# Optimization experiments

Measured on AMD Instinct MI355X. Metric: run time of the kernel, lower is better.

## Reference

```python
import jax, jax.numpy as jnp
import numpy as np

P = 399   # number of unshared per-position Conv1d kernels
K = 5     # conv kernel width (padding=2, 'same')


def _conv_stage(x, W, b):
    """Locally-connected stage: a distinct Conv1d per position along the last axis.
    x: [B, Cin, T, P]; W: [P, Cout, Cin, K]; b: [P, Cout] -> [B, Cout, T, P]."""
    xt = jnp.transpose(x, (3, 0, 1, 2))  # [P, B, Cin, T]

    def one(xi, wi, bi):
        y = jax.lax.conv_general_dilated(xi, wi, (1,), [(2, 2)],
                                         dimension_numbers=('NCH', 'OIH', 'NCH'))
        return y + bi[None, :, None]

    y = jax.vmap(one)(xt, W, b)          # [P, B, Cout, T]
    return jnp.transpose(y, (1, 2, 3, 0))


def _maxpool(x):
    # MaxPool2d((10,1), stride=(3,1)) over [B, C, T, P]
    return jax.lax.reduce_window(x, -jnp.inf, jax.lax.max,
                                 (1, 1, 10, 1), (1, 1, 3, 1), 'VALID')


def setup_inputs() -> dict:
    key = jax.random.key(0)
    ks = jax.random.split(key, 32)
    B, T = 256, 365

    def rn(k, shape, scale):
        return jax.random.normal(k, shape, jnp.float32) * scale

    d = {}
    d['x'] = jax.random.normal(ks[0], (B, T, P), jnp.float32)
    d['x2'] = jax.random.normal(ks[1], (B, 1307), jnp.float32)
    # per-position conv weights (PyTorch Conv1d layout O,I,K, stacked over P)
    d['W1'] = rn(ks[2], (P, 3, 1, K), 0.3); d['b1'] = rn(ks[3], (P, 3), 0.05)
    d['W2'] = rn(ks[4], (P, 3, 3, K), 0.2); d['b2'] = rn(ks[5], (P, 3), 0.05)
    d['W3'] = rn(ks[6], (P, 3, 3, K), 0.2); d['b3'] = rn(ks[7], (P, 3), 0.05)
    d['W4'] = rn(ks[8], (P, 3, 3, K), 0.2); d['b4'] = rn(ks[9], (P, 3), 0.05)
    # self.layers: 1307 -> 700 -> 200 -> 100
    d['lW1'] = rn(ks[10], (1307, 700), 0.02); d['lb1'] = rn(ks[11], (700,), 0.01)
    d['lW2'] = rn(ks[12], (700, 200), 0.03);  d['lb2'] = rn(ks[13], (200,), 0.01)
    d['lW3'] = rn(ks[14], (200, 100), 0.05);  d['lb3'] = rn(ks[15], (100,), 0.01)
    # self.common_layers: 1297 -> 500 -> 100 -> 20
    d['cW1'] = rn(ks[16], (1297, 500), 0.02); d['cb1'] = rn(ks[17], (500,), 0.01)
    d['cW2'] = rn(ks[18], (500, 100), 0.04);  d['cb2'] = rn(ks[19], (100,), 0.01)
    d['cW3'] = rn(ks[20], (100, 20), 0.08);   d['cb3'] = rn(ks[21], (20,), 0.01)
    # last_layer: 20 -> 1
    d['fW'] = rn(ks[22], (20, 1), 0.2);       d['fb'] = rn(ks[23], (1,), 0.01)
    return d


def reference(x, x2, W1, b1, W2, b2, W3, b3, W4, b4,
              lW1, lb1, lW2, lb2, lW3, lb3,
              cW1, cb1, cW2, cb2, cW3, cb3, fW, fb):
    h = x[:, None, :, :]                       # [B, 1, T, P]
    for W, b in ((W1, b1), (W2, b2), (W3, b3), (W4, b4)):
        h = _maxpool(jax.nn.relu(_conv_stage(h, W, b)))
    enc1 = h.reshape(h.shape[0], -1)           # [B, 3*1*399] = [B, 1197]

    e = jax.nn.relu(x2 @ lW1 + lb1)
    e = jax.nn.relu(e @ lW2 + lb2)
    enc2 = e @ lW3 + lb3                       # [B, 100] (no ReLU on final Linear)

    c = jnp.concatenate([enc1, enc2], axis=1)  # [B, 1297]
    c = jax.nn.relu(c @ cW1 + cb1)
    c = jax.nn.relu(c @ cW2 + cb2)
    c = jax.nn.relu(c @ cW3 + cb3)
    return c @ fW + fb                         # [B, 1]
```

## Files before the change

kernel.cpp:

```cpp
#include <hip/hip_runtime.h>

#define PP 399
#define BB 256


template<int SEG>
__device__ __forceinline__ float xload(const float* __restrict__ inp, int idx) {
    if (SEG == 2) {
        int ic = idx < 364 ? idx : 364;
        float v = inp[(long)ic * PP];
        return (idx <= 364) ? v : 0.f;
    }
    return inp[(long)idx * PP];
}

template<int OFF>
__device__ __forceinline__ void s1_group(const float (&xv)[13],
    const float (&w1)[3][5], const float (&B1)[3],
    float (&A1)[3], float (&c0)[3])
{
#pragma unroll
    for (int co = 0; co < 3; ++co) {
        float a0 = B1[co], a1 = B1[co], a2 = B1[co];
#pragma unroll
        for (int t = 0; t < 5; ++t) {
            a0 = fmaf(xv[OFF + t],     w1[co][t], a0);
            a1 = fmaf(xv[OFF + 1 + t], w1[co][t], a1);
            a2 = fmaf(xv[OFF + 2 + t], w1[co][t], a2);
        }
        c0[co] = a0;
        A1[co] = fmaxf(fmaxf(a0, a1), a2);
    }
}

template<int P2>
__device__ __forceinline__ void s2_step(
    float (&fe)[3][4], const float (&e)[3],
    const float (&w2)[3][3][5], const float (&B2)[3],
    float (&A2a)[3], float (&A2b)[3], float (&A2c)[3], float (&A2cur)[3],
    float*& op, bool do_c2, bool do_emit)
{
    if (do_c2) {
        float c2v[3];
#pragma unroll
        for (int co = 0; co < 3; ++co) {
            float a = B2[co];
#pragma unroll
            for (int ci = 0; ci < 3; ++ci) {
                a = fmaf(fe[ci][0], w2[co][ci][0], a);
                a = fmaf(fe[ci][1], w2[co][ci][1], a);
                a = fmaf(fe[ci][2], w2[co][ci][2], a);
                a = fmaf(fe[ci][3], w2[co][ci][3], a);
                a = fmaf(e[ci],     w2[co][ci][4], a);
            }
            c2v[co] = a;
        }
        if (P2 == 0) {
#pragma unroll
            for (int co = 0; co < 3; ++co) { A2a[co] = A2b[co]; A2b[co] = A2c[co]; A2c[co] = A2cur[co]; }
            if (do_emit) {
#pragma unroll
                for (int co = 0; co < 3; ++co)
                    op[co * PP] = fmaxf(fmaxf(fmaxf(fmaxf(A2a[co], A2b[co]), A2c[co]), c2v[co]), 0.f);
                op += 3 * PP;
            }
#pragma unroll
            for (int co = 0; co < 3; ++co) A2cur[co] = c2v[co];
        } else {
#pragma unroll
            for (int co = 0; co < 3; ++co) A2cur[co] = fmaxf(A2cur[co], c2v[co]);
        }
    }
#pragma unroll
    for (int ci = 0; ci < 3; ++ci) {
        fe[ci][0] = fe[ci][1]; fe[ci][1] = fe[ci][2]; fe[ci][2] = fe[ci][3]; fe[ci][3] = e[ci];
    }
}

template<int P2>
__device__ __forceinline__ void emit_e(
    const float (&Aa)[3], const float (&Ab)[3], const float (&Ac)[3],
    const float (&c0)[3],
    float (&fe)[3][4],
    const float (&w2)[3][3][5], const float (&B2)[3],
    float (&A2a)[3], float (&A2b)[3], float (&A2c)[3], float (&A2cur)[3],
    float*& op, bool do_c2, bool do_emit)
{
    float e[3];
#pragma unroll
    for (int co = 0; co < 3; ++co)
        e[co] = fmaxf(fmaxf(fmaxf(fmaxf(Aa[co], Ab[co]), Ac[co]), c0[co]), 0.f);
    s2_step<P2>(fe, e, w2, B2, A2a, A2b, A2c, A2cur, op, do_c2, do_emit);
}

template<int SEG>
__device__ __forceinline__ void s12_body(
    const float* __restrict__ x,
    const float* __restrict__ W1, const float* __restrict__ b1,
    const float* __restrict__ W2, const float* __restrict__ b2,
    float* __restrict__ h2, int b, int p)
{
    constexpr int J0tab[4] = {0, 13, 25, 37};
    constexpr int j0 = J0tab[SEG];
    constexpr int j1 = J0tab[SEG + 1];
    constexpr int k0 = (SEG == 0) ? 0 : 3 * j0 - 2;
    constexpr int kend = (3 * j1 + 11 < 121) ? (3 * j1 + 11) : 121;
    constexpr int NGRP = kend - k0 + 1;
    constexpr int NS = NGRP / 3;
    constexpr int NREM = NGRP - 3 * NS;
    constexpr int c2start = (SEG == 0) ? 5 : (k0 + 7);
    constexpr int e2start = 3 * j0 + 14;
    constexpr int P2_0 = (SEG == 0) ? 1 : 2;
    constexpr int P2_1 = (SEG == 0) ? 2 : 0;
    constexpr int P2_2 = (SEG == 0) ? 0 : 1;

    float w1[3][5], B1[3];
    {
        const float* wp = W1 + (long)p * 15;
#pragma unroll
        for (int co = 0; co < 3; ++co) {
#pragma unroll
            for (int t = 0; t < 5; ++t) w1[co][t] = wp[co * 5 + t];
            B1[co] = b1[(long)p * 3 + co];
        }
    }
    float w2[3][3][5], B2[3];
    {
        const float* wp = W2 + (long)p * 45;
#pragma unroll
        for (int co = 0; co < 3; ++co) {
#pragma unroll
            for (int ci = 0; ci < 3; ++ci)
#pragma unroll
                for (int t = 0; t < 5; ++t) w2[co][ci][t] = wp[(co * 3 + ci) * 5 + t];
            B2[co] = b2[(long)p * 3 + co];
        }
    }

    const float* __restrict__ inp = x + (long)b * 365 * PP + p;
    float* op = h2 + ((long)b * 37 + j0) * 3 * PP + p;

    float xv[13];
#pragma unroll
    for (int s = 0; s < 13; ++s) {
        int idx = 3 * k0 - 2 + s;
        xv[s] = (idx >= 0) ? inp[(long)idx * PP] : 0.f;
    }

    float fe[3][4];
    float A1p[3][3];
    float A2a[3], A2b[3], A2c[3], A2cur[3];
#pragma unroll
    for (int ci = 0; ci < 3; ++ci)
#pragma unroll
        for (int s = 0; s < 4; ++s) fe[ci][s] = 0.f;
#pragma unroll
    for (int co = 0; co < 3; ++co) {
        A1p[0][co] = 0.f; A1p[1][co] = 0.f; A1p[2][co] = 0.f;
        A2a[co] = 0.f; A2b[co] = 0.f; A2c[co] = 0.f; A2cur[co] = 0.f;
    }

    for (int S = 0; S < NS; ++S) {
        int k = k0 + 3 * S;
        float q[9];
#pragma unroll
        for (int s = 0; s < 9; ++s)
            q[s] = xload<SEG>(inp, 3 * k + 11 + s);

        float A1c0[3], A1c1[3], A1c2[3], c0[3];

        s1_group<0>(xv, w1, B1, A1c0, c0);
        if (S >= 1)
            emit_e<P2_0>(A1p[0], A1p[1], A1p[2], c0, fe, w2, B2,
                         A2a, A2b, A2c, A2cur, op,
                         k >= c2start, k >= e2start);
        s1_group<3>(xv, w1, B1, A1c1, c0);
        if (S >= 1)
            emit_e<P2_1>(A1p[1], A1p[2], A1c0, c0, fe, w2, B2,
                         A2a, A2b, A2c, A2cur, op,
                         k + 1 >= c2start, k + 1 >= e2start);
        s1_group<6>(xv, w1, B1, A1c2, c0);
        if (S >= 1)
            emit_e<P2_2>(A1p[2], A1c0, A1c1, c0, fe, w2, B2,
                         A2a, A2b, A2c, A2cur, op,
                         k + 2 >= c2start, k + 2 >= e2start);

#pragma unroll
        for (int co = 0; co < 3; ++co) {
            A1p[0][co] = A1c0[co]; A1p[1][co] = A1c1[co]; A1p[2][co] = A1c2[co];
        }
        xv[0] = xv[9]; xv[1] = xv[10]; xv[2] = xv[11]; xv[3] = xv[12];
#pragma unroll
        for (int s = 0; s < 9; ++s) xv[4 + s] = q[s];
    }

    if constexpr (NREM >= 1) {
        int k = k0 + 3 * NS;
        float A1c0[3], c0[3];
        s1_group<0>(xv, w1, B1, A1c0, c0);
        emit_e<P2_0>(A1p[0], A1p[1], A1p[2], c0, fe, w2, B2,
                     A2a, A2b, A2c, A2cur, op,
                     k >= c2start, k >= e2start);
        if constexpr (NREM >= 2) {
            float A1c1[3];
            s1_group<3>(xv, w1, B1, A1c1, c0);
            emit_e<P2_1>(A1p[1], A1p[2], A1c0, c0, fe, w2, B2,
                         A2a, A2b, A2c, A2cur, op,
                         k + 1 >= c2start, k + 1 >= e2start);
        }
    }
    if constexpr (SEG == 2) {
        float ez[3] = {0.f, 0.f, 0.f};
        s2_step<0>(fe, ez, w2, B2, A2a, A2b, A2c, A2cur, op, true, true);
    }
}

template<int RELU_A>
__device__ __forceinline__ void gemm_tile(
    const float* __restrict__ A, const float* __restrict__ Wt,
    float* __restrict__ out, int K, int N, int lda, int ldo, int kchunk,
    int bx, int by, int bz)
{
    __shared__ float As[32][36];
    __shared__ float Bs[32][36];

    int tid = threadIdx.x;
    int ty  = tid >> 3;
    int tx4 = (tid & 7) * 4;
    int c0 = bx * 32;
    int m0 = by * 32;
    int k0 = bz * kchunk;
    int klim = min(K, k0 + kchunk);

    float4 acc = make_float4(0.f, 0.f, 0.f, 0.f);

    for (int kb = k0; kb < klim; kb += 32) {
#pragma unroll
        for (int j = 0; j < 4; ++j) {
            int kk = kb + tx4 + j;
            float v = (kk < klim) ? A[(long)(m0 + ty) * lda + kk] : 0.f;
            if (RELU_A) v = fmaxf(v, 0.f);
            As[ty][tx4 + j] = v;
        }
#pragma unroll
        for (int j = 0; j < 4; ++j) {
            int kk = kb + ty;
            int c = c0 + tx4 + j;
            Bs[ty][tx4 + j] = (kk < klim && c < N) ? Wt[(long)kk * N + c] : 0.f;
        }
        __syncthreads();
#pragma unroll
        for (int kk = 0; kk < 32; ++kk) {
            float a = As[ty][kk];
            float4 bv = *(const float4*)&Bs[kk][tx4];
            acc.x = fmaf(a, bv.x, acc.x);
            acc.y = fmaf(a, bv.y, acc.y);
            acc.z = fmaf(a, bv.z, acc.z);
            acc.w = fmaf(a, bv.w, acc.w);
        }
        __syncthreads();
    }

    long m = m0 + ty;
    if (c0 + tx4 + 0 < N) atomicAdd(&out[m * ldo + c0 + tx4 + 0], acc.x);
    if (c0 + tx4 + 1 < N) atomicAdd(&out[m * ldo + c0 + tx4 + 1], acc.y);
    if (c0 + tx4 + 2 < N) atomicAdd(&out[m * ldo + c0 + tx4 + 2], acc.z);
    if (c0 + tx4 + 3 < N) atomicAdd(&out[m * ldo + c0 + tx4 + 3], acc.w);
}

template<int RELU_A>
__global__ __launch_bounds__(256)
void gemm_atomic(const float* __restrict__ A, const float* __restrict__ Wt,
                 float* __restrict__ out, int K, int N, int lda, int ldo, int kchunk)
{
    gemm_tile<RELU_A>(A, Wt, out, K, N, lda, ldo, kchunk,
                      blockIdx.x, blockIdx.y, blockIdx.z);
}

__global__ __launch_bounds__(256)
void init_e1(float* __restrict__ e1, const float* __restrict__ lb1)
{
    int idx = blockIdx.x * 256 + threadIdx.x;
    if (idx < BB * 700) e1[idx] = lb1[idx % 700];
}

__global__ __launch_bounds__(256)
void d1_conv_s12_lw1(const float* __restrict__ x,
                     const float* __restrict__ W1, const float* __restrict__ b1,
                     const float* __restrict__ W2, const float* __restrict__ b2,
                     float* __restrict__ h2,
                     const float* __restrict__ x2, const float* __restrict__ lW1,
                     float* __restrict__ e1,
                     float* __restrict__ e2,  const float* __restrict__ lb2,
                     float* __restrict__ cbuf, const float* __restrict__ lb3,
                     float* __restrict__ c1,  const float* __restrict__ cb1,
                     float* __restrict__ c2,  const float* __restrict__ cb2,
                     float* __restrict__ c3b, const float* __restrict__ cb3)
{
    int blk = blockIdx.x;
    if (blk < 1197) {
        int seg = blk / 399;
        int bx  = blk - seg * 399;
        int gid = bx * 256 + threadIdx.x;
        int b = gid / PP;
        int p = gid - b * PP;
        if (seg == 0)      s12_body<0>(x, W1, b1, W2, b2, h2, b, p);
        else if (seg == 1) s12_body<1>(x, W1, b1, W2, b2, h2, b, p);
        else               s12_body<2>(x, W1, b1, W2, b2, h2, b, p);
    } else if (blk < 1197 + 1056) {
        int g = blk - 1197;
        int gx = g % 22;
        int gy = (g / 22) % 8;
        int gz = g / 176;
        gemm_tile<0>(x2, lW1, e1, 1307, 700, 1307, 700, 256, gx, gy, gz);
    } else {
        int idx = (blk - 2253) * 256 + threadIdx.x;
        if (idx < BB * 200) { e2[idx] = lb2[idx % 200]; return; }
        idx -= BB * 200;
        if (idx < BB * 100) { int m = idx / 100, c = idx % 100; cbuf[(long)m * 1297 + 1197 + c] = lb3[c]; return; }
        idx -= BB * 100;
        if (idx < BB * 500) { c1[idx] = cb1[idx % 500]; return; }
        idx -= BB * 500;
        if (idx < BB * 100) { c2[idx] = cb2[idx % 100]; return; }
        idx -= BB * 100;
        if (idx < BB * 20)  { c3b[idx] = cb3[idx % 20]; return; }
    }
}

template<int CIN>
struct Stage {
    float w[3][CIN][5];
    float b[3];
    float xw[CIN][5];
    float m1[3], m2[3], m3[3];
    int nin;
};

__device__ __forceinline__ void init_s3(Stage<3>& s, const float* __restrict__ Wt,
                                        const float* __restrict__ Bs, int p) {
    const float* wp = Wt + (long)p * 45;
#pragma unroll
    for (int co = 0; co < 3; ++co)
#pragma unroll
        for (int ci = 0; ci < 3; ++ci)
#pragma unroll
            for (int k = 0; k < 5; ++k)
                s.w[co][ci][k] = wp[(co * 3 + ci) * 5 + k];
#pragma unroll
    for (int co = 0; co < 3; ++co) s.b[co] = Bs[(long)p * 3 + co];
#pragma unroll
    for (int ci = 0; ci < 3; ++ci)
#pragma unroll
        for (int k = 0; k < 5; ++k) s.xw[ci][k] = 0.f;
#pragma unroll
    for (int co = 0; co < 3; ++co) { s.m1[co] = -1e30f; s.m2[co] = -1e30f; s.m3[co] = -1e30f; }
    s.nin = 0;
}

template<int CIN>
__device__ __forceinline__ bool feed(Stage<CIN>& s, const float* in, float* out) {
#pragma unroll
    for (int ci = 0; ci < CIN; ++ci) {
        s.xw[ci][0] = s.xw[ci][1];
        s.xw[ci][1] = s.xw[ci][2];
        s.xw[ci][2] = s.xw[ci][3];
        s.xw[ci][3] = s.xw[ci][4];
        s.xw[ci][4] = in[ci];
    }
    int t = s.nin - 2;
    s.nin++;
    if (t < 0) return false;

    float c[3];
#pragma unroll
    for (int co = 0; co < 3; ++co) {
        float a = s.b[co];
#pragma unroll
        for (int ci = 0; ci < CIN; ++ci)
#pragma unroll
            for (int k = 0; k < 5; ++k)
                a = fmaf(s.xw[ci][k], s.w[co][ci][k], a);
        c[co] = fmaxf(a, 0.f);
    }

    bool emit = false;
    int ph = t % 3;
    if (ph == 0) {
        if (t >= 9) {
#pragma unroll
            for (int co = 0; co < 3; ++co) out[co] = fmaxf(s.m1[co], c[co]);
            emit = true;
        }
#pragma unroll
        for (int co = 0; co < 3; ++co) {
            float a = fmaxf(s.m2[co], c[co]);
            float bb = fmaxf(s.m3[co], c[co]);
            s.m1[co] = a; s.m2[co] = bb; s.m3[co] = c[co];
        }
    } else {
#pragma unroll
        for (int co = 0; co < 3; ++co) {
            s.m1[co] = fmaxf(s.m1[co], c[co]);
            s.m2[co] = fmaxf(s.m2[co], c[co]);
            s.m3[co] = fmaxf(s.m3[co], c[co]);
        }
    }
    return emit;
}

__device__ __forceinline__ void s34_body(
    const float* __restrict__ h2,
    const float* __restrict__ W3, const float* __restrict__ b3,
    const float* __restrict__ W4, const float* __restrict__ b4,
    float* __restrict__ cbuf, int b, int p)
{
    Stage<3> s3, s4;
    init_s3(s3, W3, b3, p);
    init_s3(s4, W4, b4, p);

    const float* inp = h2 + (long)b * 37 * 3 * PP + p;
    float* o4 = cbuf + (long)b * 1297 + p;

    float v3[3], v4[3];
    float z[3] = {0.f, 0.f, 0.f};

    float r0[3], r1[3], r2[3], r3[3], r4[3];
#pragma unroll
    for (int ci = 0; ci < 3; ++ci) {
        r0[ci] = inp[(long)(0 * 3 + ci) * PP];
        r1[ci] = inp[(long)(1 * 3 + ci) * PP];
        r2[ci] = inp[(long)(2 * 3 + ci) * PP];
        r3[ci] = inp[(long)(3 * 3 + ci) * PP];
        r4[ci] = inp[(long)(4 * 3 + ci) * PP];
    }

    for (int i = 0; i < 39; ++i) {
        float nn[3];
        int i5 = i + 5;
#pragma unroll
        for (int ci = 0; ci < 3; ++ci)
            nn[ci] = (i5 < 37) ? inp[(long)(i5 * 3 + ci) * PP] : 0.f;
        if (feed(s3, r0, v3)) {
            if (feed(s4, v3, v4)) {
#pragma unroll
                for (int co = 0; co < 3; ++co) o4[co * PP] = v4[co];
            }
        }
#pragma unroll
        for (int ci = 0; ci < 3; ++ci) {
            r0[ci] = r1[ci]; r1[ci] = r2[ci]; r2[ci] = r3[ci]; r3[ci] = r4[ci]; r4[ci] = nn[ci];
        }
    }
    for (int r = 0; r < 2; ++r) {
        if (feed(s4, z, v4)) {
#pragma unroll
            for (int co = 0; co < 3; ++co) o4[co * PP] = v4[co];
        }
    }
}

__global__ __launch_bounds__(256)
void d2_conv_s34_lw2(const float* __restrict__ h2,
                     const float* __restrict__ W3, const float* __restrict__ b3,
                     const float* __restrict__ W4, const float* __restrict__ b4,
                     float* __restrict__ cbuf,
                     const float* __restrict__ e1, const float* __restrict__ lW2,
                     float* __restrict__ e2)
{
    int blk = blockIdx.x;
    if (blk < 399) {
        int gid = blk * 256 + threadIdx.x;
        int b = gid / PP;
        int p = gid - b * PP;
        s34_body(h2, W3, b3, W4, b4, cbuf, b, p);
    } else {
        int g = blk - 399;
        int gx = g % 7;
        int gy = (g / 7) % 8;
        int gz = g / 56;
        gemm_tile<1>(e1, lW2, e2, 700, 200, 700, 200, 128, gx, gy, gz);
    }
}

__global__ __launch_bounds__(256)
void d3_lw3_cw1a(const float* __restrict__ e2, const float* __restrict__ lW3,
                 float* __restrict__ cbuf,
                 const float* __restrict__ cW1, float* __restrict__ c1)
{
    int blk = blockIdx.x;
    if (blk < 128) {
        int gx = blk % 4;
        int gy = (blk / 4) % 8;
        int gz = blk / 32;
        gemm_tile<1>(e2, lW3, cbuf + 1197, 200, 100, 200, 1297, 64, gx, gy, gz);
    } else {
        int g = blk - 128;
        int gx = g % 16;
        int gy = (g / 16) % 8;
        int gz = g / 128;
        gemm_tile<0>(cbuf, cW1, c1, 1197, 500, 1297, 500, 200, gx, gy, gz);
    }
}

__global__ __launch_bounds__(64)
void final_kernel(const float* __restrict__ c3,
                  const float* __restrict__ fW,
                  const float* __restrict__ fb,
                  float* __restrict__ out)
{
    int m = blockIdx.x * 64 + threadIdx.x;
    if (m >= BB) return;
    float acc = fb[0];
#pragma unroll
    for (int k = 0; k < 20; ++k)
        acc = fmaf(fmaxf(c3[m * 20 + k], 0.f), fW[k], acc);
    out[m] = acc;
}

extern "C" void kernel_launch(void* const* d_in, const int* in_sizes, int n_in,
                              void* d_out, int out_size, void* d_ws, size_t ws_size,
                              hipStream_t stream)
{
    const float* x   = (const float*)d_in[0];
    const float* x2  = (const float*)d_in[1];
    const float* W1  = (const float*)d_in[2];
    const float* b1  = (const float*)d_in[3];
    const float* W2  = (const float*)d_in[4];
    const float* b2  = (const float*)d_in[5];
    const float* W3  = (const float*)d_in[6];
    const float* b3  = (const float*)d_in[7];
    const float* W4  = (const float*)d_in[8];
    const float* b4  = (const float*)d_in[9];
    const float* lW1 = (const float*)d_in[10];
    const float* lb1 = (const float*)d_in[11];
    const float* lW2 = (const float*)d_in[12];
    const float* lb2 = (const float*)d_in[13];
    const float* lW3 = (const float*)d_in[14];
    const float* lb3 = (const float*)d_in[15];
    const float* cW1 = (const float*)d_in[16];
    const float* cb1 = (const float*)d_in[17];
    const float* cW2 = (const float*)d_in[18];
    const float* cb2 = (const float*)d_in[19];
    const float* cW3 = (const float*)d_in[20];
    const float* cb3 = (const float*)d_in[21];
    const float* fW  = (const float*)d_in[22];
    const float* fb  = (const float*)d_in[23];
    float* out = (float*)d_out;

    float* ws = (float*)d_ws;
    const long n_h2   = (long)BB * 37 * 3 * PP;
    const long n_cbuf = (long)BB * 1297;
    float* h2   = ws;
    float* cbuf = h2 + n_h2;
    float* e1   = cbuf + n_cbuf;
    float* e2   = e1 + (long)BB * 700;
    float* c1   = e2 + (long)BB * 200;
    float* c2   = c1 + (long)BB * 500;
    float* c3b  = c2 + (long)BB * 100;

    init_e1<<<700, 256, 0, stream>>>(e1, lb1);

    d1_conv_s12_lw1<<<1197 + 1056 + 920, 256, 0, stream>>>(
        x, W1, b1, W2, b2, h2, x2, lW1, e1,
        e2, lb2, cbuf, lb3, c1, cb1, c2, cb2, c3b, cb3);

    d2_conv_s34_lw2<<<399 + 336, 256, 0, stream>>>(h2, W3, b3, W4, b4, cbuf,
                                                   e1, lW2, e2);

    d3_lw3_cw1a<<<128 + 768, 256, 0, stream>>>(e2, lW3, cbuf, cW1, c1);

    gemm_atomic<0><<<dim3(16, 8, 1), 256, 0, stream>>>(cbuf + 1197, cW1 + (long)1197 * 500, c1, 100, 500, 1297, 500, 100);

    gemm_atomic<1><<<dim3( 4, 8, 8), 256, 0, stream>>>(c1, cW2, c2, 500, 100, 500, 100, 64);
    gemm_atomic<1><<<dim3( 1, 8, 4), 256, 0, stream>>>(c2, cW3, c3b, 100, 20, 100, 20, 32);

    final_kernel<<<dim3(4), 64, 0, stream>>>(c3b, fW, fb, out);
}
```

Measured before the change: 164.4 us.

## Fuse MLP tail into one per-row head kernel and split conv stage into two segments

Replaces four small launches (enc2 part of cW1, cW2, cW3 GEMMs with atomics, and the final dot) with a single head_kernel that works one batch row per block. It finishes the cW1 contribution from enc2, then runs the remaining layers through shared memory, removing launch overhead, the atomic accumulation, and the bias-initialisation writes for c2 and c3. The conv stage 1-2 work is also re-partitioned from three time segments to two, so each thread does more sequential work while fewer blocks are launched. The head kernel reads the weights per block with little reuse, and longer segments lower parallelism.

```diff
diff --git a/kernel.cpp b/kernel.cpp
--- a/kernel.cpp
+++ b/kernel.cpp
@@ -6,7 +6,7 @@
 
 template<int SEG>
 __device__ __forceinline__ float xload(const float* __restrict__ inp, int idx) {
-    if (SEG == 2) {
+    if (SEG == 1) {
         int ic = idx < 364 ? idx : 364;
         float v = inp[(long)ic * PP];
         return (idx <= 364) ? v : 0.f;
@@ -100,7 +100,7 @@
     const float* __restrict__ W2, const float* __restrict__ b2,
     float* __restrict__ h2, int b, int p)
 {
-    constexpr int J0tab[4] = {0, 13, 25, 37};
+    constexpr int J0tab[3] = {0, 19, 37};
     constexpr int j0 = J0tab[SEG];
     constexpr int j1 = J0tab[SEG + 1];
     constexpr int k0 = (SEG == 0) ? 0 : 3 * j0 - 2;
@@ -209,7 +209,7 @@
                          k + 1 >= c2start, k + 1 >= e2start);
         }
     }
-    if constexpr (SEG == 2) {
+    if constexpr (SEG == 1) {
         float ez[3] = {0.f, 0.f, 0.f};
         s2_step<0>(fe, ez, w2, B2, A2a, A2b, A2c, A2cur, op, true, true);
     }
@@ -266,15 +266,6 @@
     if (c0 + tx4 + 1 < N) atomicAdd(&out[m * ldo + c0 + tx4 + 1], acc.y);
     if (c0 + tx4 + 2 < N) atomicAdd(&out[m * ldo + c0 + tx4 + 2], acc.z);
     if (c0 + tx4 + 3 < N) atomicAdd(&out[m * ldo + c0 + tx4 + 3], acc.w);
-}
-
-template<int RELU_A>
-__global__ __launch_bounds__(256)
-void gemm_atomic(const float* __restrict__ A, const float* __restrict__ Wt,
-                 float* __restrict__ out, int K, int N, int lda, int ldo, int kchunk)
-{
-    gemm_tile<RELU_A>(A, Wt, out, K, N, lda, ldo, kchunk,
-                      blockIdx.x, blockIdx.y, blockIdx.z);
 }
 
 __global__ __launch_bounds__(256)
@@ -293,37 +284,30 @@
                      float* __restrict__ e1,
                      float* __restrict__ e2,  const float* __restrict__ lb2,
                      float* __restrict__ cbuf, const float* __restrict__ lb3,
-                     float* __restrict__ c1,  const float* __restrict__ cb1,
-                     float* __restrict__ c2,  const float* __restrict__ cb2,
-                     float* __restrict__ c3b, const float* __restrict__ cb3)
+                     float* __restrict__ c1,  const float* __restrict__ cb1)
 {
     int blk = blockIdx.x;
-    if (blk < 1197) {
+    if (blk < 798) {
         int seg = blk / 399;
         int bx  = blk - seg * 399;
         int gid = bx * 256 + threadIdx.x;
         int b = gid / PP;
         int p = gid - b * PP;
-        if (seg == 0)      s12_body<0>(x, W1, b1, W2, b2, h2, b, p);
-        else if (seg == 1) s12_body<1>(x, W1, b1, W2, b2, h2, b, p);
-        else               s12_body<2>(x, W1, b1, W2, b2, h2, b, p);
-    } else if (blk < 1197 + 1056) {
-        int g = blk - 1197;
+        if (seg == 0) s12_body<0>(x, W1, b1, W2, b2, h2, b, p);
+        else          s12_body<1>(x, W1, b1, W2, b2, h2, b, p);
+    } else if (blk < 798 + 1056) {
+        int g = blk - 798;
         int gx = g % 22;
         int gy = (g / 22) % 8;
         int gz = g / 176;
         gemm_tile<0>(x2, lW1, e1, 1307, 700, 1307, 700, 256, gx, gy, gz);
     } else {
-        int idx = (blk - 2253) * 256 + threadIdx.x;
+        int idx = (blk - 1854) * 256 + threadIdx.x;
         if (idx < BB * 200) { e2[idx] = lb2[idx % 200]; return; }
         idx -= BB * 200;
         if (idx < BB * 100) { int m = idx / 100, c = idx % 100; cbuf[(long)m * 1297 + 1197 + c] = lb3[c]; return; }
         idx -= BB * 100;
         if (idx < BB * 500) { c1[idx] = cb1[idx % 500]; return; }
-        idx -= BB * 500;
-        if (idx < BB * 100) { c2[idx] = cb2[idx % 100]; return; }
-        idx -= BB * 100;
-        if (idx < BB * 20)  { c3b[idx] = cb3[idx % 20]; return; }
     }
 }
 
@@ -502,19 +486,73 @@
     }
 }
 
-__global__ __launch_bounds__(64)
-void final_kernel(const float* __restrict__ c3,
-                  const float* __restrict__ fW,
-                  const float* __restrict__ fb,
-                  float* __restrict__ out)
-{
-    int m = blockIdx.x * 64 + threadIdx.x;
-    if (m >= BB) return;
-    float acc = fb[0];
-#pragma unroll
-    for (int k = 0; k < 20; ++k)
-        acc = fmaf(fmaxf(c3[m * 20 + k], 0.f), fW[k], acc);
-    out[m] = acc;
+__global__ __launch_bounds__(256)
+void head_kernel(const float* __restrict__ c1,
+                 const float* __restrict__ cbuf,
+                 const float* __restrict__ cW1b,
+                 const float* __restrict__ cW2, const float* __restrict__ cb2,
+                 const float* __restrict__ cW3, const float* __restrict__ cb3,
+                 const float* __restrict__ fW, const float* __restrict__ fb,
+                 float* __restrict__ out)
+{
+    __shared__ float enc2s[100];
+    __shared__ float c1s[500];
+    __shared__ float c2s[100];
+    __shared__ float c3s[20];
+    int m = blockIdx.x;
+    int t = threadIdx.x;
+
+    if (t < 100) enc2s[t] = cbuf[(long)m * 1297 + 1197 + t];
+    __syncthreads();
+
+    if (t < 250) {
+        int col = 2 * t;
+        float a0 = c1[(long)m * 500 + col];
+        float a1 = c1[(long)m * 500 + col + 1];
+#pragma unroll 4
+        for (int k = 0; k < 100; ++k) {
+            float ev = enc2s[k];
+            a0 = fmaf(ev, cW1b[(long)k * 500 + col], a0);
+            a1 = fmaf(ev, cW1b[(long)k * 500 + col + 1], a1);
+        }
+        c1s[col]     = fmaxf(a0, 0.f);
+        c1s[col + 1] = fmaxf(a1, 0.f);
+    }
+    __syncthreads();
+
+    if (t < 100) {
+        float a0 = cb2[t], a1 = 0.f, a2 = 0.f, a3 = 0.f;
+#pragma unroll 4
+        for (int k = 0; k < 500; k += 4) {
+            a0 = fmaf(c1s[k],     cW2[(long)k * 100 + t],       a0);
+            a1 = fmaf(c1s[k + 1], cW2[(long)(k + 1) * 100 + t], a1);
+            a2 = fmaf(c1s[k + 2], cW2[(long)(k + 2) * 100 + t], a2);
+            a3 = fmaf(c1s[k + 3], cW2[(long)(k + 3) * 100 + t], a3);
+        }
+        c2s[t] = fmaxf((a0 + a1) + (a2 + a3), 0.f);
+    }
+    __syncthreads();
+
+    if (t < 20) {
+        float a0 = cb3[t], a1 = 0.f, a2 = 0.f, a3 = 0.f;
+#pragma unroll 4
+        for (int k = 0; k < 100; k += 4) {
+            a0 = fmaf(c2s[k],     cW3[(long)k * 20 + t],       a0);
+            a1 = fmaf(c2s[k + 1], cW3[(long)(k + 1) * 20 + t], a1);
+            a2 = fmaf(c2s[k + 2], cW3[(long)(k + 2) * 20 + t], a2);
+            a3 = fmaf(c2s[k + 3], cW3[(long)(k + 3) * 20 + t], a3);
+        }
+        c3s[t] = fmaxf((a0 + a1) + (a2 + a3), 0.f);
+    }
+    __syncthreads();
+
+    if (t == 0) {
+        float a = fb[0];
+#pragma unroll
+        for (int k = 0; k < 20; ++k)
+            a = fmaf(c3s[k], fW[k], a);
+        out[m] = a;
+    }
 }
 
 extern "C" void kernel_launch(void* const* d_in, const int* in_sizes, int n_in,
@@ -555,24 +593,18 @@
     float* e1   = cbuf + n_cbuf;
     float* e2   = e1 + (long)BB * 700;
     float* c1   = e2 + (long)BB * 200;
-    float* c2   = c1 + (long)BB * 500;
-    float* c3b  = c2 + (long)BB * 100;
 
     init_e1<<<700, 256, 0, stream>>>(e1, lb1);
 
-    d1_conv_s12_lw1<<<1197 + 1056 + 920, 256, 0, stream>>>(
+    d1_conv_s12_lw1<<<798 + 1056 + 800, 256, 0, stream>>>(
         x, W1, b1, W2, b2, h2, x2, lW1, e1,
-        e2, lb2, cbuf, lb3, c1, cb1, c2, cb2, c3b, cb3);
+        e2, lb2, cbuf, lb3, c1, cb1);
 
     d2_conv_s34_lw2<<<399 + 336, 256, 0, stream>>>(h2, W3, b3, W4, b4, cbuf,
                                                    e1, lW2, e2);
 
     d3_lw3_cw1a<<<128 + 768, 256, 0, stream>>>(e2, lW3, cbuf, cW1, c1);
 
-    gemm_atomic<0><<<dim3(16, 8, 1), 256, 0, stream>>>(cbuf + 1197, cW1 + (long)1197 * 500, c1, 100, 500, 1297, 500, 100);
-
-    gemm_atomic<1><<<dim3( 4, 8, 8), 256, 0, stream>>>(c1, cW2, c2, 500, 100, 500, 100, 64);
-    gemm_atomic<1><<<dim3( 1, 8, 4), 256, 0, stream>>>(c2, cW3, c3b, 100, 20, 100, 20, 32);
-
-    final_kernel<<<dim3(4), 64, 0, stream>>>(c3b, fW, fb, out);
-}
+    head_kernel<<<256, 256, 0, stream>>>(c1, cbuf, cW1 + (long)1197 * 500,
+                                         cW2, cb2, cW3, cb3, fW, fb, out);
+}
```

Result: slower. 174.0 us (+5.8%).
